# Kernel optimization log

Measured on AMD Instinct MI355X. Metric: run time of the kernel, lower is better.

Reference implementation:

```python
import jax, jax.numpy as jnp
import numpy as np
import math

K = 3          # kernel_size
P_GEM = 3.0    # GeM power
EPS_GEM = 1e-6
EPS_NORM = 1e-12


def _l2n(x, axis):
    n = jnp.sqrt(jnp.sum(x * x, axis=axis, keepdims=True))
    return x / jnp.maximum(n, EPS_NORM)


def setup_inputs() -> dict:
    key = jax.random.key(0)
    ks = jax.random.split(key, 7)
    b, hw, c, nc = 32, 196, 768, 4096
    hidden = c  # mlp_ratio = 1
    return {
        "patch_tokens": jax.random.normal(ks[0], (b, hw, c), dtype=jnp.float32),
        "fc1_w": jax.random.normal(ks[1], (c, hidden), dtype=jnp.float32) * 0.02,
        "fc1_b": jnp.zeros((hidden,), dtype=jnp.float32),
        "fc2_w": jax.random.normal(ks[2], (hidden, c), dtype=jnp.float32) * 0.02,
        "fc2_b": jnp.zeros((c,), dtype=jnp.float32),
        "head_w": jax.random.normal(ks[3], (c, nc), dtype=jnp.float32) * 0.02,
        "head_b": jnp.zeros((nc,), dtype=jnp.float32),
    }


def reference(patch_tokens, fc1_w, fc1_b, fc2_w, fc2_b, head_w, head_b):
    b, hw, c = patch_tokens.shape
    h = w = int(math.sqrt(hw))

    # ---- SpaceSelfAware: pad -> unfold (3x3 local windows) -> multiply ----
    img = jnp.transpose(patch_tokens, (0, 2, 1)).reshape(b, c, h, w)
    # ZeroPad2d((left=1, right=1, top=2, bottom=0)) for kernel_size=3
    padded = jnp.pad(img, ((0, 0), (0, 0), (K - 1, 0), (K // 2, K // 2)))
    # stack the 9 shifted views, row-major over (ki, kj) matching nn.Unfold
    wins = jnp.stack(
        [padded[:, :, ki:ki + h, kj:kj + w] for ki in range(K) for kj in range(K)],
        axis=2,
    )  # (b, c, 9, h, w)
    y = wins.reshape(b, c, K, K, hw)
    y = jnp.transpose(y, (0, 4, 1, 2, 3))  # (b, hw, c, K, K)
    ssa = patch_tokens[:, :, :, None, None] * y  # (b, hw, c, K, K)

    # ---- space_fusion: L2Norm(dim=1) then GeM(p=3) over the KxK window ----
    ssa = _l2n(ssa, axis=1)
    pooled = jnp.mean(jnp.clip(ssa, EPS_GEM, None) ** P_GEM, axis=(-2, -1)) ** (1.0 / P_GEM)  # (b, hw, c)

    # ---- residual + L2 normalize over channels + Mlp ----
    tokens = pooled + patch_tokens
    tokens = _l2n(tokens, axis=-1)
    hdn = jax.nn.gelu(tokens @ fc1_w + fc1_b, approximate=False)
    tokens = hdn @ fc2_w + fc2_b  # (b, hw, c)

    # ---- GeMHead: GeM(p=3) over tokens, linear to nc, L2 normalize ----
    g = jnp.mean(jnp.clip(tokens, EPS_GEM, None) ** P_GEM, axis=1) ** (1.0 / P_GEM)  # (b, c)
    desc = g @ head_w + head_b  # (b, nc)
    desc = _l2n(desc, axis=-1)
    return desc
```

## Files before the change

kernel.cpp:

```cpp
#include <hip/hip_runtime.h>
#include <hip/hip_bf16.h>
#include <math.h>

#define B   32
#define P   196
#define C   768
#define NC  4096
#define HH  14
#define KSPLIT 12
#define NT  12
#define M6  6272
#define TW  (768 * 32)
#define TM  (M6 * 32)

typedef _Float16 half8 __attribute__((ext_vector_type(8)));
typedef _Float16 half4 __attribute__((ext_vector_type(4)));
typedef float f32x4 __attribute__((ext_vector_type(4)));

#define GLOAD_LDS16(g, l)                                                      \
    __builtin_amdgcn_global_load_lds(                                          \
        (const __attribute__((address_space(1))) void*)(g),                    \
        (__attribute__((address_space(3))) void*)(l), 16, 0, 0)

__global__ __launch_bounds__(256) void k_ssa(const float* __restrict__ t,
                                             _Float16* __restrict__ outP,
                                             float* __restrict__ partial) {
    const int b = blockIdx.y, cb = blockIdx.x, c0 = cb * 16;
    __shared__ float xp_[256 * 16];
    __shared__ float part[4][9][16];
    __shared__ float inv_norm[9][16];
    __shared__ _Float16 outT[P][16];
    const int tid = threadIdx.x;
    const int cc = tid & 15, g = tid >> 4, wv = tid >> 6;

#pragma unroll
    for (int q = 0; q < 16; ++q) xp_[q * 256 + tid] = 0.0f;
    __syncthreads();

    for (int idx = tid; idx < 784; idx += 256) {
        const int p = idx >> 2, c = (idx & 3) * 4;
        const int i = p / HH, j = p % HH;
        *(float4*)&xp_[((i + 2) * 16 + (j + 1)) * 16 + c] =
            *(const float4*)&t[((size_t)b * P + p) * C + c0 + c];
    }
    __syncthreads();

    float s[9] = {};
    {
        int i = 0, j = g;
        if (j >= HH) { j -= HH; i = 1; }
        for (int p = g; p < P; p += 16) {
            const int base = ((i + 2) * 16 + (j + 1)) * 16 + cc;
            const float xp = xp_[base];
            const float xp2 = xp * xp;
#pragma unroll
            for (int k = 0; k < 9; ++k) {
                const int off = ((k / 3) - 2) * 16 + (k % 3) - 1;
                const float nb = xp_[base + off * 16];
                s[k] += xp2 * nb * nb;
            }
            j += 2; ++i;
            if (j >= HH) { j -= HH; ++i; }
        }
    }
#pragma unroll
    for (int k = 0; k < 9; ++k) {
        float r = s[k];
        r += __shfl_xor(r, 16);
        r += __shfl_xor(r, 32);
        s[k] = r;
    }
    if ((tid & 63) < 16) {
#pragma unroll
        for (int k = 0; k < 9; ++k) part[wv][k][cc] = s[k];
    }
    __syncthreads();
    if (tid < 144) {
        const int k = tid >> 4, c2 = tid & 15;
        const float t4 = part[0][k][c2] + part[1][k][c2] +
                         part[2][k][c2] + part[3][k][c2];
        inv_norm[k][c2] = 1.0f / fmaxf(sqrtf(t4), 1e-12f);
    }
    __syncthreads();

    float invn[9];
#pragma unroll
    for (int k = 0; k < 9; ++k) invn[k] = inv_norm[k][cc];

    {
        int i = 0, j = g;
        if (j >= HH) { j -= HH; i = 1; }
        for (int p = g; p < P; p += 16) {
            const int base = ((i + 2) * 16 + (j + 1)) * 16 + cc;
            const float xp = xp_[base];
            float acc = 0.0f;
#pragma unroll
            for (int k = 0; k < 9; ++k) {
                const int off = ((k / 3) - 2) * 16 + (k % 3) - 1;
                const float v = xp * xp_[base + off * 16];
                const float u = fmaxf(v * invn[k], 1e-6f);
                acc += u * u * u;
            }
            const float val = cbrtf(acc * (1.0f / 9.0f)) + xp;
            float rs = val * val;
            rs += __shfl_xor(rs, 1);
            rs += __shfl_xor(rs, 2);
            rs += __shfl_xor(rs, 4);
            rs += __shfl_xor(rs, 8);
            outT[p][cc] = (_Float16)val;
            if (cc == 0) partial[(size_t)cb * M6 + b * P + p] = rs;
            j += 2; ++i;
            if (j >= HH) { j -= HH; ++i; }
        }
    }
    __syncthreads();
    const int kb = cb >> 1, kbase = (cb & 1) * 16;
    for (int idx = tid; idx < P * 2; idx += 256) {
        const int p = idx >> 1, h = idx & 1;
        const half8 v = *(const half8*)&outT[p][h * 8];
        const int row = b * P + p;
        const int slot = ((kbase + h * 8) >> 3) ^ ((row >> 1) & 3);
        *(half8*)&outP[(size_t)kb * TM + (size_t)row * 32 + slot * 8] = v;
    }
}

__global__ __launch_bounds__(256) void k_prep(const float* __restrict__ W1,
                                              const float* __restrict__ W2,
                                              _Float16* __restrict__ O1,
                                              _Float16* __restrict__ O2,
                                              const float* __restrict__ spart,
                                              float* __restrict__ invv) {
    if (blockIdx.z == 2) {
        const int row = (blockIdx.y * 24 + blockIdx.x) * 256 + threadIdx.x;
        if (row < M6) {
            float s = 0.0f;
#pragma unroll 8
            for (int cb = 0; cb < 48; ++cb) s += spart[(size_t)cb * M6 + row];
            invv[row] = 1.0f / fmaxf(sqrtf(s), 1e-12f);
        }
        return;
    }
    const float* W = blockIdx.z ? W2 : W1;
    _Float16* WtP = blockIdx.z ? O2 : O1;
    __shared__ float tt[32][33];
    const int k0 = blockIdx.x * 32, n0 = blockIdx.y * 32;
    const int r = threadIdx.x / 32, c = threadIdx.x % 32;
#pragma unroll
    for (int q = 0; q < 4; ++q)
        tt[r + q * 8][c] = W[(size_t)(k0 + r + q * 8) * C + n0 + c];
    __syncthreads();
    const int nl = threadIdx.x >> 3, h = threadIdx.x & 7;
    const int n = n0 + nl;
    half4 v;
#pragma unroll
    for (int j = 0; j < 4; ++j) v[j] = (_Float16)tt[h * 4 + j][nl];
    const int el = (h * 4) ^ (((n >> 1) & 3) << 3);
    *(half4*)&WtP[(size_t)blockIdx.x * TW + (size_t)n * 32 + el] = v;
}

template <bool GELU>
__global__ __launch_bounds__(256) void k_mfma_gemm(
    const _Float16* __restrict__ TokP,
    const _Float16* __restrict__ WtP,
    const float* __restrict__ bias,
    const float* __restrict__ invv,
    _Float16* __restrict__ Cout,
    float* __restrict__ gpart) {
    __shared__ _Float16 lA[3][2][64][32];
    __shared__ _Float16 lB[3][2][64][32];
    __shared__ float part2[2][2][64];
    const int tid = threadIdx.x;
    const int w = tid >> 6, l = tid & 63;
    const int l15 = l & 15, lk = l >> 4;

    const int lid = blockIdx.x;
    int vm, vn;
    if (lid < 1152) { vm = (lid / 96) * 8 + (lid & 7); vn = (lid % 96) >> 3; }
    else            { const int r = lid - 1152; vm = 96 + r / 12; vn = r % 12; }
    const int m0 = vm * 64, n0 = vn * 64;
    const int wn = (w & 1) * 32, wm = (w >> 1) * 32;

    f32x4 acc[2][2] = {};

    const int kbsel = w & 1;
    const bool isB = (w >= 2);
    const _Float16* srcBase =
        isB ? (TokP + (size_t)m0 * 32) : (WtP + (size_t)n0 * 32);
    const size_t tileStride = isB ? (size_t)TM : (size_t)TW;
    _Float16* dst0 = isB ? &lB[0][kbsel][0][0] : &lA[0][kbsel][0][0];

#define ISSUE(tt, bf_)                                                         \
    {   const _Float16* s_ = srcBase + (size_t)(2 * (tt) + kbsel) * tileStride;\
        _Float16* d_ = dst0 + (size_t)(bf_) * 4096;                            \
        GLOAD_LDS16(s_ + l * 8,        d_ + l * 8);                            \
        GLOAD_LDS16(s_ + 512 + l * 8,  d_ + 512 + l * 8);                      \
        GLOAD_LDS16(s_ + 1024 + l * 8, d_ + 1024 + l * 8);                     \
        GLOAD_LDS16(s_ + 1536 + l * 8, d_ + 1536 + l * 8); }

    ISSUE(0, 0); ISSUE(1, 1); ISSUE(2, 2);

    for (int t = 0; t < NT; ++t) {
        if (t < NT - 2)       asm volatile("s_waitcnt vmcnt(8)" ::: "memory");
        else if (t == NT - 2) asm volatile("s_waitcnt vmcnt(4)" ::: "memory");
        else                  asm volatile("s_waitcnt vmcnt(0)" ::: "memory");
        __builtin_amdgcn_s_barrier();
        __builtin_amdgcn_sched_barrier(0);

        const int buf = t % 3;
#pragma unroll
        for (int kk = 0; kk < 2; ++kk) {
            half8 af[2], bf[2];
#pragma unroll
            for (int fa = 0; fa < 2; ++fa) {
                const int rowA = wn + fa * 16 + l15;
                const int colA = (lk ^ ((rowA >> 1) & 3)) * 8;
                af[fa] = *(const half8*)&lA[buf][kk][rowA][colA];
            }
#pragma unroll
            for (int fb = 0; fb < 2; ++fb) {
                const int rowB = wm + fb * 16 + l15;
                const int colB = (lk ^ ((rowB >> 1) & 3)) * 8;
                bf[fb] = *(const half8*)&lB[buf][kk][rowB][colB];
            }
#pragma unroll
            for (int fa = 0; fa < 2; ++fa)
#pragma unroll
                for (int fb = 0; fb < 2; ++fb)
                    acc[fa][fb] = __builtin_amdgcn_mfma_f32_16x16x32_f16(
                        af[fa], bf[fb], acc[fa][fb], 0, 0, 0);
        }
        asm volatile("s_waitcnt lgkmcnt(0)" ::: "memory");
        __builtin_amdgcn_s_barrier();
        __builtin_amdgcn_sched_barrier(0);
        if (t < NT - 3) ISSUE(t + 3, buf);
    }
#undef ISSUE

    const int b0 = m0 / P;
    const int rsplit = (b0 + 1) * P;
    float invm[2];
    if constexpr (GELU) {
#pragma unroll
        for (int fb = 0; fb < 2; ++fb)
            invm[fb] = invv[m0 + wm + fb * 16 + l15];
    }
#pragma unroll
    for (int fa = 0; fa < 2; ++fa) {
        const int nb = n0 + wn + fa * 16 + lk * 4;
        const float4 bv = *(const float4*)&bias[nb];
        if constexpr (GELU) {
#pragma unroll
            for (int fb = 0; fb < 2; ++fb) {
                const int m = m0 + wm + fb * 16 + l15;
                half4 o;
#pragma unroll
                for (int rr = 0; rr < 4; ++rr) {
                    float v = acc[fa][fb][rr] * invm[fb] + ((const float*)&bv)[rr];
                    v = 0.5f * v * (1.0f + erff(v * 0.70710678118654752f));
                    o[rr] = (_Float16)v;
                }
                const int el = (nb & 31) ^ (((m >> 1) & 3) << 3);
                *(half4*)&Cout[(size_t)(nb >> 5) * TM + (size_t)m * 32 + el] = o;
            }
        } else {
#pragma unroll
            for (int rr = 0; rr < 4; ++rr) {
                float s0 = 0.0f, s1 = 0.0f;
#pragma unroll
                for (int fb = 0; fb < 2; ++fb) {
                    const int m = m0 + wm + fb * 16 + l15;
                    const float v = acc[fa][fb][rr] + ((const float*)&bv)[rr];
                    const float u = fmaxf(v, 1e-6f);
                    const float u3 = u * u * u;
                    if (m >= rsplit) s1 += u3; else s0 += u3;
                }
                s0 += __shfl_xor(s0, 1); s0 += __shfl_xor(s0, 2);
                s0 += __shfl_xor(s0, 4); s0 += __shfl_xor(s0, 8);
                s1 += __shfl_xor(s1, 1); s1 += __shfl_xor(s1, 2);
                s1 += __shfl_xor(s1, 4); s1 += __shfl_xor(s1, 8);
                if (l15 == 0) {
                    part2[w >> 1][0][wn + fa * 16 + lk * 4 + rr] = s0;
                    part2[w >> 1][1][wn + fa * 16 + lk * 4 + rr] = s1;
                }
            }
        }
    }
    if constexpr (!GELU) {
        __syncthreads();
        if (tid < 128) {
            const int seg = tid >> 6, nn = tid & 63;
            const float tot = part2[0][seg][nn] + part2[1][seg][nn];
            if (seg == 0) {
                const int q = vm - ((b0 * 49) >> 4);
                gpart[((size_t)b0 * 4 + q) * C + n0 + nn] = tot;
            } else if (rsplit < m0 + 64) {
                gpart[((size_t)(b0 + 1) * 4 + 0) * C + n0 + nn] = tot;
            }
        }
    }
}

__global__ __launch_bounds__(256) void k_gempool2(const float* __restrict__ gpart,
                                                  float* __restrict__ g) {
    const int b = blockIdx.x / 3;
    const int c = (blockIdx.x % 3) * 256 + threadIdx.x;
    const float s = gpart[((size_t)b * 4 + 0) * C + c] +
                    gpart[((size_t)b * 4 + 1) * C + c] +
                    gpart[((size_t)b * 4 + 2) * C + c] +
                    gpart[((size_t)b * 4 + 3) * C + c];
    g[b * C + c] = cbrtf(s * (1.0f / (float)P));
}

__global__ __launch_bounds__(256) void k_head1(const float* __restrict__ g,
                                               const float* __restrict__ W,
                                               float* __restrict__ partial) {
    const int n0 = blockIdx.x * 64;
    const int k0 = blockIdx.y * 64;
    __shared__ float gs[32][64];
    __shared__ float part[4][32][64];
    const int tid = threadIdx.x;

    for (int idx = tid; idx < 32 * 64; idx += 256)
        gs[idx >> 6][idx & 63] = g[(idx >> 6) * C + k0 + (idx & 63)];
    __syncthreads();

    const int c = tid & 63, q = tid >> 6;
    float acc[32] = {};
#pragma unroll
    for (int kk = 0; kk < 16; ++kk) {
        const int k = q * 16 + kk;
        const float wv = W[(size_t)(k0 + k) * NC + n0 + c];
#pragma unroll
        for (int b = 0; b < 32; ++b) acc[b] += gs[b][k] * wv;
    }
#pragma unroll
    for (int b = 0; b < 32; ++b) part[q][b][c] = acc[b];
    __syncthreads();

    for (int o = tid; o < 32 * 64; o += 256) {
        const int b = o >> 6, cc = o & 63;
        const float v = part[0][b][cc] + part[1][b][cc] +
                        part[2][b][cc] + part[3][b][cc];
        partial[((size_t)blockIdx.y * 32 + b) * NC + n0 + cc] = v;
    }
}

__global__ __launch_bounds__(256) void k_head2(const float* __restrict__ partial,
                                               const float* __restrict__ hb,
                                               float* __restrict__ out) {
    const int n = blockIdx.x * 256 + threadIdx.x;
    const int b = blockIdx.y;
    float s = hb[n];
#pragma unroll
    for (int ks = 0; ks < KSPLIT; ++ks)
        s += partial[((size_t)ks * 32 + b) * NC + n];
    out[(size_t)b * NC + n] = s;
}

__global__ __launch_bounds__(256) void k_outnorm(float* __restrict__ out) {
    const int b = blockIdx.x;
    float* r = out + (size_t)b * NC;
    const int tid = threadIdx.x;
    float v[16];
    float s = 0.0f;
#pragma unroll
    for (int q = 0; q < 16; ++q) {
        v[q] = r[tid + q * 256];
        s += v[q] * v[q];
    }
    __shared__ float partial[4];
    __shared__ float inv;
#pragma unroll
    for (int off = 32; off > 0; off >>= 1) s += __shfl_xor(s, off);
    if ((tid & 63) == 0) partial[tid >> 6] = s;
    __syncthreads();
    if (tid == 0)
        inv = 1.0f / fmaxf(sqrtf(partial[0] + partial[1] + partial[2] + partial[3]), 1e-12f);
    __syncthreads();
#pragma unroll
    for (int q = 0; q < 16; ++q) r[tid + q * 256] = v[q] * inv;
}

extern "C" void kernel_launch(void* const* d_in, const int* in_sizes, int n_in,
                              void* d_out, int out_size, void* d_ws, size_t ws_size,
                              hipStream_t stream) {
    const float* patch  = (const float*)d_in[0];
    const float* fc1_w  = (const float*)d_in[1];
    const float* fc1_b  = (const float*)d_in[2];
    const float* fc2_w  = (const float*)d_in[3];
    const float* fc2_b  = (const float*)d_in[4];
    const float* head_w = (const float*)d_in[5];
    const float* head_b = (const float*)d_in[6];
    float* out = (float*)d_out;

    const size_t big = (size_t)B * P * C;
    _Float16* tokU  = (_Float16*)d_ws;
    _Float16* hdnP  = tokU + big;
    _Float16* wt1   = hdnP + big;
    _Float16* wt2   = wt1 + C * C;
    float*    spart = (float*)(wt2 + C * C);
    float*    invv  = spart + 48 * (size_t)M6;
    float*    gbuf  = invv + M6;
    float*    gpart = gbuf + B * C;
    float*    hpart = gpart + (size_t)B * 4 * C;

    k_ssa<<<dim3(48, B), dim3(256), 0, stream>>>(patch, tokU, spart);
    k_prep<<<dim3(C / 32, C / 32, 3), dim3(256), 0, stream>>>(
        fc1_w, fc2_w, wt1, wt2, spart, invv);
    k_mfma_gemm<true><<<dim3(1176), dim3(256), 0, stream>>>(
        tokU, wt1, fc1_b, invv, hdnP, nullptr);
    k_mfma_gemm<false><<<dim3(1176), dim3(256), 0, stream>>>(
        hdnP, wt2, fc2_b, nullptr, nullptr, gpart);
    k_gempool2<<<dim3(B * 3), dim3(256), 0, stream>>>(gpart, gbuf);
    k_head1<<<dim3(NC / 64, KSPLIT), dim3(256), 0, stream>>>(gbuf, head_w, hpart);
    k_head2<<<dim3(NC / 256, B), dim3(256), 0, stream>>>(hpart, head_b, out);
    k_outnorm<<<dim3(B), dim3(256), 0, stream>>>(out);
}
```

Baseline: 82.59 us.

## Double-buffer GEMM LDS and fuse GeM pooling and head reduction kernels

The MFMA GEMM drops from a triple-buffered LDS pipeline to double buffering, prefetching two tiles ahead instead of three. The intent is to cut LDS use per block and allow higher occupancy, at the cost of less latency hiding. The final GeM cube-root step is folded into the head GEMM's input staging. The split-K head reduction is merged with the output L2 normalization, which removes two kernel launches and a global round trip. The merged head2 kernel runs only 32 blocks, one per batch row, so that stage gets less parallelism.

Measured after the change: 126.7 us. 1.53x slower.

```diff
diff --git a/kernel.cpp b/kernel.cpp
--- a/kernel.cpp
+++ b/kernel.cpp
@@ -166,8 +166,8 @@
     const float* __restrict__ invv,
     _Float16* __restrict__ Cout,
     float* __restrict__ gpart) {
-    __shared__ _Float16 lA[3][2][64][32];
-    __shared__ _Float16 lB[3][2][64][32];
+    __shared__ _Float16 lA[2][2][64][32];
+    __shared__ _Float16 lB[2][2][64][32];
     __shared__ float part2[2][2][64];
     const int tid = threadIdx.x;
     const int w = tid >> 6, l = tid & 63;
@@ -189,24 +189,23 @@
     const size_t tileStride = isB ? (size_t)TM : (size_t)TW;
     _Float16* dst0 = isB ? &lB[0][kbsel][0][0] : &lA[0][kbsel][0][0];
 
-#define ISSUE(tt, bf_)                                                         \
+#define ISSUE(tt, st_)                                                         \
     {   const _Float16* s_ = srcBase + (size_t)(2 * (tt) + kbsel) * tileStride;\
-        _Float16* d_ = dst0 + (size_t)(bf_) * 4096;                            \
+        _Float16* d_ = dst0 + (size_t)(st_) * 4096;                            \
         GLOAD_LDS16(s_ + l * 8,        d_ + l * 8);                            \
         GLOAD_LDS16(s_ + 512 + l * 8,  d_ + 512 + l * 8);                      \
         GLOAD_LDS16(s_ + 1024 + l * 8, d_ + 1024 + l * 8);                     \
         GLOAD_LDS16(s_ + 1536 + l * 8, d_ + 1536 + l * 8); }
 
-    ISSUE(0, 0); ISSUE(1, 1); ISSUE(2, 2);
+    ISSUE(0, 0); ISSUE(1, 1);
 
     for (int t = 0; t < NT; ++t) {
-        if (t < NT - 2)       asm volatile("s_waitcnt vmcnt(8)" ::: "memory");
-        else if (t == NT - 2) asm volatile("s_waitcnt vmcnt(4)" ::: "memory");
-        else                  asm volatile("s_waitcnt vmcnt(0)" ::: "memory");
+        if (t < NT - 1) asm volatile("s_waitcnt vmcnt(4)" ::: "memory");
+        else            asm volatile("s_waitcnt vmcnt(0)" ::: "memory");
         __builtin_amdgcn_s_barrier();
         __builtin_amdgcn_sched_barrier(0);
 
-        const int buf = t % 3;
+        const int st = t & 1;
 #pragma unroll
         for (int kk = 0; kk < 2; ++kk) {
             half8 af[2], bf[2];
@@ -214,13 +213,13 @@
             for (int fa = 0; fa < 2; ++fa) {
                 const int rowA = wn + fa * 16 + l15;
                 const int colA = (lk ^ ((rowA >> 1) & 3)) * 8;
-                af[fa] = *(const half8*)&lA[buf][kk][rowA][colA];
+                af[fa] = *(const half8*)&lA[st][kk][rowA][colA];
             }
 #pragma unroll
             for (int fb = 0; fb < 2; ++fb) {
                 const int rowB = wm + fb * 16 + l15;
                 const int colB = (lk ^ ((rowB >> 1) & 3)) * 8;
-                bf[fb] = *(const half8*)&lB[buf][kk][rowB][colB];
+                bf[fb] = *(const half8*)&lB[st][kk][rowB][colB];
             }
 #pragma unroll
             for (int fa = 0; fa < 2; ++fa)
@@ -232,7 +231,7 @@
         asm volatile("s_waitcnt lgkmcnt(0)" ::: "memory");
         __builtin_amdgcn_s_barrier();
         __builtin_amdgcn_sched_barrier(0);
-        if (t < NT - 3) ISSUE(t + 3, buf);
+        if (t < NT - 2) ISSUE(t + 2, st);
     }
 #undef ISSUE
 
@@ -300,18 +299,7 @@
     }
 }
 
-__global__ __launch_bounds__(256) void k_gempool2(const float* __restrict__ gpart,
-                                                  float* __restrict__ g) {
-    const int b = blockIdx.x / 3;
-    const int c = (blockIdx.x % 3) * 256 + threadIdx.x;
-    const float s = gpart[((size_t)b * 4 + 0) * C + c] +
-                    gpart[((size_t)b * 4 + 1) * C + c] +
-                    gpart[((size_t)b * 4 + 2) * C + c] +
-                    gpart[((size_t)b * 4 + 3) * C + c];
-    g[b * C + c] = cbrtf(s * (1.0f / (float)P));
-}
-
-__global__ __launch_bounds__(256) void k_head1(const float* __restrict__ g,
+__global__ __launch_bounds__(256) void k_head1(const float* __restrict__ gpart,
                                                const float* __restrict__ W,
                                                float* __restrict__ partial) {
     const int n0 = blockIdx.x * 64;
@@ -320,8 +308,12 @@
     __shared__ float part[4][32][64];
     const int tid = threadIdx.x;
 
-    for (int idx = tid; idx < 32 * 64; idx += 256)
-        gs[idx >> 6][idx & 63] = g[(idx >> 6) * C + k0 + (idx & 63)];
+    for (int idx = tid; idx < 32 * 64; idx += 256) {
+        const int b = idx >> 6, kk = idx & 63;
+        const float* gp = &gpart[((size_t)b * 4) * C + k0 + kk];
+        const float s = gp[0] + gp[C] + gp[2 * C] + gp[3 * C];
+        gs[b][kk] = cbrtf(s * (1.0f / (float)P));
+    }
     __syncthreads();
 
     const int c = tid & 63, q = tid >> 6;
@@ -345,38 +337,33 @@
     }
 }
 
-__global__ __launch_bounds__(256) void k_head2(const float* __restrict__ partial,
-                                               const float* __restrict__ hb,
-                                               float* __restrict__ out) {
-    const int n = blockIdx.x * 256 + threadIdx.x;
-    const int b = blockIdx.y;
-    float s = hb[n];
-#pragma unroll
-    for (int ks = 0; ks < KSPLIT; ++ks)
-        s += partial[((size_t)ks * 32 + b) * NC + n];
-    out[(size_t)b * NC + n] = s;
-}
-
-__global__ __launch_bounds__(256) void k_outnorm(float* __restrict__ out) {
+__global__ __launch_bounds__(256) void k_head2n(const float* __restrict__ partial,
+                                                const float* __restrict__ hb,
+                                                float* __restrict__ out) {
     const int b = blockIdx.x;
-    float* r = out + (size_t)b * NC;
     const int tid = threadIdx.x;
     float v[16];
-    float s = 0.0f;
+    float ss = 0.0f;
 #pragma unroll
     for (int q = 0; q < 16; ++q) {
-        v[q] = r[tid + q * 256];
-        s += v[q] * v[q];
-    }
-    __shared__ float partial[4];
+        const int n = tid + q * 256;
+        float s = hb[n];
+#pragma unroll
+        for (int ks = 0; ks < KSPLIT; ++ks)
+            s += partial[((size_t)ks * 32 + b) * NC + n];
+        v[q] = s;
+        ss += s * s;
+    }
+    __shared__ float psum[4];
     __shared__ float inv;
 #pragma unroll
-    for (int off = 32; off > 0; off >>= 1) s += __shfl_xor(s, off);
-    if ((tid & 63) == 0) partial[tid >> 6] = s;
+    for (int off = 32; off > 0; off >>= 1) ss += __shfl_xor(ss, off);
+    if ((tid & 63) == 0) psum[tid >> 6] = ss;
     __syncthreads();
     if (tid == 0)
-        inv = 1.0f / fmaxf(sqrtf(partial[0] + partial[1] + partial[2] + partial[3]), 1e-12f);
-    __syncthreads();
+        inv = 1.0f / fmaxf(sqrtf(psum[0] + psum[1] + psum[2] + psum[3]), 1e-12f);
+    __syncthreads();
+    float* r = out + (size_t)b * NC;
 #pragma unroll
     for (int q = 0; q < 16; ++q) r[tid + q * 256] = v[q] * inv;
 }
@@ -400,8 +387,7 @@
     _Float16* wt2   = wt1 + C * C;
     float*    spart = (float*)(wt2 + C * C);
     float*    invv  = spart + 48 * (size_t)M6;
-    float*    gbuf  = invv + M6;
-    float*    gpart = gbuf + B * C;
+    float*    gpart = invv + M6;
     float*    hpart = gpart + (size_t)B * 4 * C;
 
     k_ssa<<<dim3(48, B), dim3(256), 0, stream>>>(patch, tokU, spart);
@@ -411,8 +397,7 @@
         tokU, wt1, fc1_b, invv, hdnP, nullptr);
     k_mfma_gemm<false><<<dim3(1176), dim3(256), 0, stream>>>(
         hdnP, wt2, fc2_b, nullptr, nullptr, gpart);
-    k_gempool2<<<dim3(B * 3), dim3(256), 0, stream>>>(gpart, gbuf);
-    k_head1<<<dim3(NC / 64, KSPLIT), dim3(256), 0, stream>>>(gbuf, head_w, hpart);
-    k_head2<<<dim3(NC / 256, B), dim3(256), 0, stream>>>(hpart, head_b, out);
-    k_outnorm<<<dim3(B), dim3(256), 0, stream>>>(out);
-}
+    k_head1<<<dim3(NC / 64, KSPLIT), dim3(256), 0, stream>>>(
+        gpart, head_w, hpart);
+    k_head2n<<<dim3(B), dim3(256), 0, stream>>>(hpart, head_b, out);
+}
```
